# Kernel optimization log

Measured on AMD Instinct MI355X. Metric: run time of the kernel, lower is better.

Reference implementation:

```python
import jax, jax.numpy as jnp
from jax import lax
import numpy as np

C = 64      # channels
K = 3       # dynamic kernel size
N = 2       # batch
H = 256
W = 256
DOWN = 4    # avgpool factor


def _conv(x, w, b):
    # 'SAME' padding matches get_same_padding for odd kernels, dilation=1
    y = lax.conv_general_dilated(x, w, (1, 1), 'SAME',
                                 dimension_numbers=('NCHW', 'OIHW', 'NCHW'))
    return y + b[None, :, None, None]


def _resblock(x, w1, b1, w2, b2):
    out = jax.nn.leaky_relu(_conv(x, w1, b1), 0.1)
    return _conv(out, w2, b2) + x


def _block(x, ws1, bs1, ws2, bs2):
    # fixed small loop over 3 structurally distinct ResBlocks
    for i in range(ws1.shape[0]):
        x = _resblock(x, ws1[i], bs1[i], ws2[i], bs2[i])
    return x


def _avgpool(x, k):
    n, c, h, w = x.shape
    return x.reshape(n, c, h // k, k, w // k, k).mean(axis=(3, 5))


def _maxpool(x, k):
    n, c, h, w = x.shape
    return x.reshape(n, c, h // k, k, w // k, k).max(axis=(3, 5))


def _dyn_conv(x, wt, k):
    # per-pixel depthwise conv: out[n,c,h,w] = sum_{dh,dw} xpad[n,c,h+dh,w+dw] * wt[n, c*k*k + dh*k + dw, h, w]
    # (torch's unfold/permute flattening pairs feat tap (dh,dw) with kernel channel index dh*k+dw)
    n, c, h, w = x.shape
    pad = (k - 1) // 2
    xp = jnp.pad(x, ((0, 0), (0, 0), (pad, pad), (pad, pad)), mode='edge')  # replicate pad
    wr = wt.reshape(n, c, k * k, h, w)
    out = jnp.zeros_like(x)
    for dh in range(k):            # fixed 3x3 tap loop; avoids materializing the unfold tensor
        for dw in range(k):
            out = out + xp[:, :, dh:dh + h, dw:dw + w] * wr[:, :, dh * k + dw]
    return out


def setup_inputs() -> dict:
    key = jax.random.key(0)
    ks = jax.random.split(key, 11)
    s = 0.05  # small init so 6 residual blocks stay numerically tame
    return {
        'x': jax.random.normal(ks[0], (N, C, H, W), jnp.float32),
        'blk1_w1': jax.random.normal(ks[1], (3, C, C, K, K), jnp.float32) * s,
        'blk1_b1': jnp.zeros((3, C), jnp.float32),
        'blk1_w2': jax.random.normal(ks[2], (3, C, C, K, K), jnp.float32) * s,
        'blk1_b2': jnp.zeros((3, C), jnp.float32),
        'blk2_w1': jax.random.normal(ks[3], (3, C, C, K, K), jnp.float32) * s,
        'blk2_b1': jnp.zeros((3, C), jnp.float32),
        'blk2_w2': jax.random.normal(ks[4], (3, C, C, K, K), jnp.float32) * s,
        'blk2_b2': jnp.zeros((3, C), jnp.float32),
        'tok_w': jax.random.normal(ks[5], (K * K * C, C, 1, 1), jnp.float32) * s,
        'tok_b': jnp.zeros((K * K * C,), jnp.float32),
    }


def reference(x, blk1_w1, blk1_b1, blk1_w2, blk1_b2,
              blk2_w1, blk2_b1, blk2_w2, blk2_b2, tok_w, tok_b):
    y = _avgpool(x, DOWN)                                   # [N,C,H/4,W/4]
    y = _block(y, blk1_w1, blk1_b1, blk1_w2, blk1_b2)
    y = _maxpool(y, 2)                                      # [N,C,H/8,W/8]
    y = _block(y, blk2_w1, blk2_b1, blk2_w2, blk2_b2)
    wt = _conv(y, tok_w, tok_b)                             # [N,9C,H/8,W/8]
    n, ck2, hs, ws = wt.shape
    # F.interpolate(scale_factor=2*down, mode='bilinear', align_corners=False)
    wt = jax.image.resize(wt, (n, ck2, hs * 2 * DOWN, ws * 2 * DOWN), method='bilinear')
    return _dyn_conv(x, wt, K)
```

## Files before the change

### kernel.cpp

```cpp
#include <hip/hip_runtime.h>


__global__ __launch_bounds__(256) void avgpool4_k(const float* __restrict__ x,
                                                  float* __restrict__ y) {
    int idx = blockIdx.x * 256 + threadIdx.x;
    int wo = idx & 63;
    int ho = (idx >> 6) & 63;
    int cz = idx >> 12;
    const float* base = x + ((long)cz * 256 + ho * 4) * 256 + wo * 4;
    float s = 0.f;
#pragma unroll
    for (int r = 0; r < 4; ++r) {
        float4 v = *(const float4*)(base + r * 256);
        s += v.x + v.y + v.z + v.w;
    }
    y[idx] = s * 0.0625f;
}

template <int S, int CIB>
__global__ __launch_bounds__(256) void conv3x3s_k(
    const float* __restrict__ in, const float* __restrict__ wgt,
    float* __restrict__ outp) {
    constexpr int KSN = 64 / CIB;
    constexpr int TPS = S / 16;
    constexpr int NT = TPS * TPS;
    constexpr int TOT = CIB * 324;
    constexpr int NLD = (TOT + 255) / 256;
    constexpr int TAIL = TOT - (NLD - 1) * 256;
    __shared__ float s_in[CIB * 360];
    __shared__ __align__(16) float s_w[CIB * 144];

    const int tid = threadIdx.x;
    int z = blockIdx.x;
    const int ks = z % KSN; z /= KSN;
    const int ocg = z & 3; z >>= 2;
    const int tile = z % NT;
    const int n = z / NT;
    const int th = (tile / TPS) * 16, tw = (tile % TPS) * 16;
    const int oc0 = ocg * 16;

    for (int i = tid; i < CIB * 144; i += 256) {
        int k = i / (CIB * 9);
        int rem = i - k * (CIB * 9);
        s_w[rem * 16 + k] = wgt[(oc0 + k) * 576 + ks * (CIB * 9) + rem];
    }

    const float* inb = in + ((long)n * 64 + ks * CIB) * (S * S);
#pragma unroll
    for (int j = 0; j < NLD; ++j) {
        int idx = tid + j * 256;
        bool slot = (j < NLD - 1) || (tid < TAIL);
        int t = slot ? idx : 0;
        int ci = t / 324;
        int rem = t - ci * 324;
        int r = rem / 18;
        int c = rem - r * 18;
        int gh = th + r - 1, gw = tw + c - 1;
        float v = 0.f;
        if (slot && (unsigned)gh < (unsigned)S && (unsigned)gw < (unsigned)S)
            v = inb[ci * (S * S) + gh * S + gw];
        if (slot) s_in[ci * 360 + r * 20 + c] = v;
    }
    __syncthreads();

    const int lane = tid & 63;
    const int wid = tid >> 6;
    const int tx4 = (lane & 3) * 4;
    const int ty = lane >> 2;

    float acc[4][4];
#pragma unroll
    for (int k = 0; k < 4; ++k)
#pragma unroll
        for (int p = 0; p < 4; ++p) acc[k][p] = 0.f;

#pragma unroll 2
    for (int ci = 0; ci < CIB; ++ci) {
        float xr[3][6];
#pragma unroll
        for (int r = 0; r < 3; ++r) {
            const float* rp = &s_in[ci * 360 + (ty + r) * 20 + tx4];
            float4 a = *(const float4*)rp;
            float2 b = *(const float2*)(rp + 4);
            xr[r][0] = a.x; xr[r][1] = a.y; xr[r][2] = a.z;
            xr[r][3] = a.w; xr[r][4] = b.x; xr[r][5] = b.y;
        }
#pragma unroll
        for (int dh = 0; dh < 3; ++dh)
#pragma unroll
            for (int dw = 0; dw < 3; ++dw) {
                float4 wv = *(const float4*)&s_w[(ci * 9 + dh * 3 + dw) * 16 + wid * 4];
#pragma unroll
                for (int p = 0; p < 4; ++p) {
                    float xv = xr[dh][p + dw];
                    acc[0][p] += xv * wv.x;
                    acc[1][p] += xv * wv.y;
                    acc[2][p] += xv * wv.z;
                    acc[3][p] += xv * wv.w;
                }
            }
    }

    const int gy = th + ty, gx = tw + tx4;
    const long pstride = (long)2 * 64 * S * S;
#pragma unroll
    for (int k = 0; k < 4; ++k) {
        float4 v;
        v.x = acc[k][0]; v.y = acc[k][1]; v.z = acc[k][2]; v.w = acc[k][3];
        long off = ks * pstride +
                   ((long)(n * 64 + oc0 + wid * 4 + k)) * (S * S) + gy * S + gx;
        *(float4*)&outp[off] = v;
    }
}

template <int NP, int SSLOG, bool LRELU, bool RES>
__global__ __launch_bounds__(256) void comb_k(
    const float* __restrict__ P, const float* __restrict__ bias,
    const float* __restrict__ res, float* __restrict__ out) {
    const long pstride = (long)2 * 64 << SSLOG;
    long base = ((long)blockIdx.x * 256 + threadIdx.x) * 4;
    int c = (int)((base >> SSLOG) & 63);
    float4 v = *(const float4*)&P[base];
#pragma unroll
    for (int p = 1; p < NP; ++p) {
        float4 u = *(const float4*)&P[base + p * pstride];
        v.x += u.x; v.y += u.y; v.z += u.z; v.w += u.w;
    }
    float b = bias[c];
    v.x += b; v.y += b; v.z += b; v.w += b;
    if (LRELU) {
        v.x = v.x > 0.f ? v.x : 0.1f * v.x;
        v.y = v.y > 0.f ? v.y : 0.1f * v.y;
        v.z = v.z > 0.f ? v.z : 0.1f * v.z;
        v.w = v.w > 0.f ? v.w : 0.1f * v.w;
    }
    if (RES) {
        float4 r = *(const float4*)&res[base];
        v.x += r.x; v.y += r.y; v.z += r.z; v.w += r.w;
    }
    *(float4*)&out[base] = v;
}

__global__ __launch_bounds__(256) void maxpool_comb_k(
    const float* __restrict__ Pb, const float* __restrict__ bias,
    const float* __restrict__ res, float* __restrict__ P) {
    int idx = blockIdx.x * 256 + threadIdx.x;
    int wo = idx & 31;
    int ho = (idx >> 5) & 31;
    int cz = idx >> 10;
    float bch = bias[cz & 63];
    float m = -3.4e38f;
#pragma unroll
    for (int dh = 0; dh < 2; ++dh)
#pragma unroll
        for (int dw = 0; dw < 2; ++dw) {
            long off = ((long)cz * 64 + ho * 2 + dh) * 64 + wo * 2 + dw;
            float y = Pb[off] + Pb[off + 524288] + Pb[off + 1048576] +
                      Pb[off + 1572864] + bch + res[off];
            m = fmaxf(m, y);
        }
    P[idx] = m;
}

__global__ __launch_bounds__(256) void conv1x1_k(
    const float* __restrict__ in, const float* __restrict__ w,
    const float* __restrict__ b, float* __restrict__ out) {
    __shared__ float s_in[32 * 256];
    __shared__ __align__(16) float s_w[64 * 8];
    const int tid = threadIdx.x;
    const int p0 = blockIdx.x * 256;
    const int cog = blockIdx.y;
    const int n = blockIdx.z;

    for (int idx = tid; idx < 512; idx += 256) {
        int j = idx >> 6;
        int ci = idx & 63;
        s_w[ci * 8 + j] = w[(long)cog * 512 + idx];
    }

    float acc[8];
#pragma unroll
    for (int i = 0; i < 8; ++i) acc[i] = b[cog * 8 + i];

    float pf[32];
#pragma unroll
    for (int i = 0; i < 32; ++i)
        pf[i] = in[(long)(n * 64 + i) * 1024 + p0 + tid];

    for (int chunk = 0; chunk < 64; chunk += 32) {
        __syncthreads();
#pragma unroll
        for (int i = 0; i < 32; ++i) s_in[i * 256 + tid] = pf[i];
        __syncthreads();
        if (chunk + 32 < 64) {
#pragma unroll
            for (int i = 0; i < 32; ++i)
                pf[i] = in[(long)(n * 64 + chunk + 32 + i) * 1024 + p0 + tid];
        }
#pragma unroll 4
        for (int ci = 0; ci < 32; ++ci) {
            float v = s_in[ci * 256 + tid];
            float4 w0 = *(const float4*)&s_w[(chunk + ci) * 8];
            float4 w1 = *(const float4*)&s_w[(chunk + ci) * 8 + 4];
            acc[0] += v * w0.x; acc[1] += v * w0.y;
            acc[2] += v * w0.z; acc[3] += v * w0.w;
            acc[4] += v * w1.x; acc[5] += v * w1.y;
            acc[6] += v * w1.z; acc[7] += v * w1.w;
        }
    }
#pragma unroll
    for (int oc = 0; oc < 8; ++oc)
        out[(long)(n * 576 + cog * 8 + oc) * 1024 + p0 + tid] = acc[oc];
}

__global__ __launch_bounds__(256) void dynconv_k(
    const float* __restrict__ x, const float* __restrict__ wt,
    float* __restrict__ out) {
    __shared__ __align__(16) float s_x[10 * 132];
    const int tid = threadIdx.x;
    const int tx = tid & 31;
    const int ty = tid >> 5;
    const int tw = (blockIdx.x & 1) * 128;
    const int th = (blockIdx.x >> 1) * 8;
    const int cz = blockIdx.y;

    const float* xb = x + (long)cz * 65536;
    for (int idx = tid; idx < 1300; idx += 256) {
        int r = idx / 130;
        int c = idx - r * 130;
        int gh = min(max(th + r - 1, 0), 255);
        int gw = min(max(tw + c - 1, 0), 255);
        s_x[r * 132 + c] = xb[gh * 256 + gw];
    }

    const int h = th + ty;
    const int wbase = tw + tx * 4;

    float src_h = h * 0.125f - 0.4375f;
    int h0 = (int)floorf(src_h);
    float fh = src_h - (float)h0;
    int h0c = min(max(h0, 0), 31), h1c = min(max(h0 + 1, 0), 31);
    float src_w = wbase * 0.125f - 0.4375f;
    int w0 = (int)floorf(src_w);
    float fw0 = src_w - (float)w0;
    int w0c = min(max(w0, 0), 31), w1c = min(max(w0 + 1, 0), 31);

    __syncthreads();

    float vals[3][6];
#pragma unroll
    for (int r = 0; r < 3; ++r) {
        const float* rp = &s_x[(ty + r) * 132 + tx * 4];
        float4 a = *(const float4*)rp;
        float2 b = *(const float2*)(rp + 4);
        vals[r][0] = a.x; vals[r][1] = a.y; vals[r][2] = a.z;
        vals[r][3] = a.w; vals[r][4] = b.x; vals[r][5] = b.y;
    }

    const float* wtb = wt + (long)cz * 9 * 1024;
    float acc[4] = {0.f, 0.f, 0.f, 0.f};
#pragma unroll
    for (int dh = 0; dh < 3; ++dh)
#pragma unroll
        for (int dw = 0; dw < 3; ++dw) {
            const float* p = wtb + (dh * 3 + dw) * 1024;
            float w00 = p[h0c * 32 + w0c], w01 = p[h0c * 32 + w1c];
            float w10 = p[h1c * 32 + w0c], w11 = p[h1c * 32 + w1c];
            float c0 = w00 + fh * (w10 - w00);
            float c1 = w01 + fh * (w11 - w01);
            float d = c1 - c0;
#pragma unroll
            for (int j = 0; j < 4; ++j) {
                float wv = c0 + (fw0 + 0.125f * j) * d;
                acc[j] += vals[dh][j + dw] * wv;
            }
        }

    float4 o;
    o.x = acc[0]; o.y = acc[1]; o.z = acc[2]; o.w = acc[3];
    *(float4*)&out[(long)cz * 65536 + h * 256 + wbase] = o;
}

extern "C" void kernel_launch(void* const* d_in, const int* in_sizes, int n_in,
                              void* d_out, int out_size, void* d_ws, size_t ws_size,
                              hipStream_t stream) {
    const float* x    = (const float*)d_in[0];
    const float* b1w1 = (const float*)d_in[1];
    const float* b1b1 = (const float*)d_in[2];
    const float* b1w2 = (const float*)d_in[3];
    const float* b1b2 = (const float*)d_in[4];
    const float* b2w1 = (const float*)d_in[5];
    const float* b2b1 = (const float*)d_in[6];
    const float* b2w2 = (const float*)d_in[7];
    const float* b2b2 = (const float*)d_in[8];
    const float* tokw = (const float*)d_in[9];
    const float* tokb = (const float*)d_in[10];
    float* out = (float*)d_out;
    float* ws = (float*)d_ws;

    float* X0 = ws;
    float* X1 = ws + 524288;
    float* T  = ws + 1048576;
    float* P  = ws + 1572864;
    float* Pm = ws + 3670016;
    float* Q  = ws + 3801088;
    float* U  = ws + 3932160;
    float* WT = ws + 4063232;

    const int WSZ = 64 * 64 * 9;

    avgpool4_k<<<2048, 256, 0, stream>>>(x, X0);

    conv3x3s_k<64, 16><<<512, 256, 0, stream>>>(X0, b1w1 + 0 * WSZ, P);
    comb_k<4, 12, true,  false><<<512, 256, 0, stream>>>(P, b1b1 + 0, nullptr, T);
    conv3x3s_k<64, 16><<<512, 256, 0, stream>>>(T, b1w2 + 0 * WSZ, P);
    comb_k<4, 12, false, true ><<<512, 256, 0, stream>>>(P, b1b2 + 0, X0, X1);

    conv3x3s_k<64, 16><<<512, 256, 0, stream>>>(X1, b1w1 + 1 * WSZ, P);
    comb_k<4, 12, true,  false><<<512, 256, 0, stream>>>(P, b1b1 + 64, nullptr, T);
    conv3x3s_k<64, 16><<<512, 256, 0, stream>>>(T, b1w2 + 1 * WSZ, P);
    comb_k<4, 12, false, true ><<<512, 256, 0, stream>>>(P, b1b2 + 64, X1, X0);

    conv3x3s_k<64, 16><<<512, 256, 0, stream>>>(X0, b1w1 + 2 * WSZ, P);
    comb_k<4, 12, true,  false><<<512, 256, 0, stream>>>(P, b1b1 + 128, nullptr, T);
    conv3x3s_k<64, 16><<<512, 256, 0, stream>>>(T, b1w2 + 2 * WSZ, P);
    maxpool_comb_k<<<512, 256, 0, stream>>>(P, b1b2 + 128, X0, Pm);

    conv3x3s_k<32, 8><<<256, 256, 0, stream>>>(Pm, b2w1 + 0 * WSZ, P);
    comb_k<8, 10, true,  false><<<128, 256, 0, stream>>>(P, b2b1 + 0, nullptr, U);
    conv3x3s_k<32, 8><<<256, 256, 0, stream>>>(U, b2w2 + 0 * WSZ, P);
    comb_k<8, 10, false, true ><<<128, 256, 0, stream>>>(P, b2b2 + 0, Pm, Q);

    conv3x3s_k<32, 8><<<256, 256, 0, stream>>>(Q, b2w1 + 1 * WSZ, P);
    comb_k<8, 10, true,  false><<<128, 256, 0, stream>>>(P, b2b1 + 64, nullptr, U);
    conv3x3s_k<32, 8><<<256, 256, 0, stream>>>(U, b2w2 + 1 * WSZ, P);
    comb_k<8, 10, false, true ><<<128, 256, 0, stream>>>(P, b2b2 + 64, Q, Pm);

    conv3x3s_k<32, 8><<<256, 256, 0, stream>>>(Pm, b2w1 + 2 * WSZ, P);
    comb_k<8, 10, true,  false><<<128, 256, 0, stream>>>(P, b2b1 + 128, nullptr, U);
    conv3x3s_k<32, 8><<<256, 256, 0, stream>>>(U, b2w2 + 2 * WSZ, P);
    comb_k<8, 10, false, true ><<<128, 256, 0, stream>>>(P, b2b2 + 128, Pm, Q);

    conv1x1_k<<<dim3(4, 72, 2), 256, 0, stream>>>(Q, tokw, tokb, WT);

    dynconv_k<<<dim3(64, 128), 256, 0, stream>>>(x, WT, out);
}
```

Measured before the change: 387.9 us.

## Widen conv tiles, deepen split-K, and stage dynconv weights in shared memory

```diff
diff --git a/kernel.cpp b/kernel.cpp
--- a/kernel.cpp
+++ b/kernel.cpp
@@ -17,17 +17,20 @@
     y[idx] = s * 0.0625f;
 }
 
-template <int S, int CIB>
-__global__ __launch_bounds__(256) void conv3x3s_k(
+template <int S, int CIB, int TW, int PXL>
+__global__ __launch_bounds__(256) void conv3x3w_k(
     const float* __restrict__ in, const float* __restrict__ wgt,
     float* __restrict__ outp) {
     constexpr int KSN = 64 / CIB;
-    constexpr int TPS = S / 16;
-    constexpr int NT = TPS * TPS;
-    constexpr int TOT = CIB * 324;
+    constexpr int TH = 16;
+    constexpr int NTW = S / TW, NTH = S / TH;
+    constexpr int NT = NTW * NTH;
+    constexpr int HW = TW + 2;
+    constexpr int SROW = TW + 4;
+    constexpr int TOT = CIB * 18 * HW;
     constexpr int NLD = (TOT + 255) / 256;
     constexpr int TAIL = TOT - (NLD - 1) * 256;
-    __shared__ float s_in[CIB * 360];
+    __shared__ float s_in[CIB * 18 * SROW];
     __shared__ __align__(16) float s_w[CIB * 144];
 
     const int tid = threadIdx.x;
@@ -36,7 +39,7 @@
     const int ocg = z & 3; z >>= 2;
     const int tile = z % NT;
     const int n = z / NT;
-    const int th = (tile / TPS) * 16, tw = (tile % TPS) * 16;
+    const int th0 = (tile / NTW) * TH, tw0 = (tile % NTW) * TW;
     const int oc0 = ocg * 16;
 
     for (int i = tid; i < CIB * 144; i += 256) {
@@ -51,39 +54,44 @@
         int idx = tid + j * 256;
         bool slot = (j < NLD - 1) || (tid < TAIL);
         int t = slot ? idx : 0;
-        int ci = t / 324;
-        int rem = t - ci * 324;
-        int r = rem / 18;
-        int c = rem - r * 18;
-        int gh = th + r - 1, gw = tw + c - 1;
+        int ci = t / (18 * HW);
+        int rem = t - ci * (18 * HW);
+        int r = rem / HW;
+        int c = rem - r * HW;
+        int gh = th0 + r - 1, gw = tw0 + c - 1;
         float v = 0.f;
         if (slot && (unsigned)gh < (unsigned)S && (unsigned)gw < (unsigned)S)
             v = inb[ci * (S * S) + gh * S + gw];
-        if (slot) s_in[ci * 360 + r * 20 + c] = v;
+        if (slot) s_in[ci * (18 * SROW) + r * SROW + c] = v;
     }
     __syncthreads();
 
     const int lane = tid & 63;
     const int wid = tid >> 6;
-    const int tx4 = (lane & 3) * 4;
-    const int ty = lane >> 2;
-
-    float acc[4][4];
+    const int lx = lane & 3;
+    const int ly = lane >> 2;
+    const int px0 = lx * PXL;
+
+    float acc[4][PXL];
 #pragma unroll
     for (int k = 0; k < 4; ++k)
 #pragma unroll
-        for (int p = 0; p < 4; ++p) acc[k][p] = 0.f;
-
-#pragma unroll 2
+        for (int p = 0; p < PXL; ++p) acc[k][p] = 0.f;
+
+#pragma unroll
     for (int ci = 0; ci < CIB; ++ci) {
-        float xr[3][6];
+        float xr[3][PXL + 2];
 #pragma unroll
         for (int r = 0; r < 3; ++r) {
-            const float* rp = &s_in[ci * 360 + (ty + r) * 20 + tx4];
-            float4 a = *(const float4*)rp;
-            float2 b = *(const float2*)(rp + 4);
-            xr[r][0] = a.x; xr[r][1] = a.y; xr[r][2] = a.z;
-            xr[r][3] = a.w; xr[r][4] = b.x; xr[r][5] = b.y;
+            const float* rp = &s_in[ci * (18 * SROW) + (ly + r) * SROW + px0];
+#pragma unroll
+            for (int q = 0; q < PXL / 4; ++q) {
+                float4 a = *(const float4*)(rp + q * 4);
+                xr[r][q * 4 + 0] = a.x; xr[r][q * 4 + 1] = a.y;
+                xr[r][q * 4 + 2] = a.z; xr[r][q * 4 + 3] = a.w;
+            }
+            float2 b = *(const float2*)(rp + PXL);
+            xr[r][PXL] = b.x; xr[r][PXL + 1] = b.y;
         }
 #pragma unroll
         for (int dh = 0; dh < 3; ++dh)
@@ -91,7 +99,7 @@
             for (int dw = 0; dw < 3; ++dw) {
                 float4 wv = *(const float4*)&s_w[(ci * 9 + dh * 3 + dw) * 16 + wid * 4];
 #pragma unroll
-                for (int p = 0; p < 4; ++p) {
+                for (int p = 0; p < PXL; ++p) {
                     float xv = xr[dh][p + dw];
                     acc[0][p] += xv * wv.x;
                     acc[1][p] += xv * wv.y;
@@ -101,15 +109,19 @@
             }
     }
 
-    const int gy = th + ty, gx = tw + tx4;
+    const int gy = th0 + ly, gx = tw0 + px0;
     const long pstride = (long)2 * 64 * S * S;
 #pragma unroll
     for (int k = 0; k < 4; ++k) {
-        float4 v;
-        v.x = acc[k][0]; v.y = acc[k][1]; v.z = acc[k][2]; v.w = acc[k][3];
         long off = ks * pstride +
                    ((long)(n * 64 + oc0 + wid * 4 + k)) * (S * S) + gy * S + gx;
-        *(float4*)&outp[off] = v;
+#pragma unroll
+        for (int q = 0; q < PXL / 4; ++q) {
+            float4 v;
+            v.x = acc[k][q * 4 + 0]; v.y = acc[k][q * 4 + 1];
+            v.z = acc[k][q * 4 + 2]; v.w = acc[k][q * 4 + 3];
+            *(float4*)&outp[off + q * 4] = v;
+        }
     }
 }
 
@@ -141,6 +153,7 @@
     *(float4*)&out[base] = v;
 }
 
+template <int NP>
 __global__ __launch_bounds__(256) void maxpool_comb_k(
     const float* __restrict__ Pb, const float* __restrict__ bias,
     const float* __restrict__ res, float* __restrict__ P) {
@@ -155,8 +168,9 @@
 #pragma unroll
         for (int dw = 0; dw < 2; ++dw) {
             long off = ((long)cz * 64 + ho * 2 + dh) * 64 + wo * 2 + dw;
-            float y = Pb[off] + Pb[off + 524288] + Pb[off + 1048576] +
-                      Pb[off + 1572864] + bch + res[off];
+            float y = bch + res[off];
+#pragma unroll
+            for (int p = 0; p < NP; ++p) y += Pb[off + (long)p * 524288];
             m = fmaxf(m, y);
         }
     P[idx] = m;
@@ -217,6 +231,7 @@
     const float* __restrict__ x, const float* __restrict__ wt,
     float* __restrict__ out) {
     __shared__ __align__(16) float s_x[10 * 132];
+    __shared__ float s_wt[9 * 60];
     const int tid = threadIdx.x;
     const int tx = tid & 31;
     const int ty = tid >> 5;
@@ -233,17 +248,31 @@
         s_x[r * 132 + c] = xb[gh * 256 + gw];
     }
 
+    const int h0min = th / 8 - 1;
+    const int w0min = tw / 8 - 1;
+    const float* wtb = wt + (long)cz * 9 * 1024;
+    for (int i = tid; i < 540; i += 256) {
+        int tap = i / 60;
+        int rem = i - tap * 60;
+        int r = rem / 20;
+        int c = rem - r * 20;
+        if (c < 18) {
+            int gr = min(max(h0min + r, 0), 31);
+            int gc = min(max(w0min + c, 0), 31);
+            s_wt[i] = wtb[tap * 1024 + gr * 32 + gc];
+        }
+    }
+
     const int h = th + ty;
     const int wbase = tw + tx * 4;
-
     float src_h = h * 0.125f - 0.4375f;
     int h0 = (int)floorf(src_h);
     float fh = src_h - (float)h0;
-    int h0c = min(max(h0, 0), 31), h1c = min(max(h0 + 1, 0), 31);
+    int r0 = h0 - h0min;
     float src_w = wbase * 0.125f - 0.4375f;
     int w0 = (int)floorf(src_w);
     float fw0 = src_w - (float)w0;
-    int w0c = min(max(w0, 0), 31), w1c = min(max(w0 + 1, 0), 31);
+    int j = w0 - w0min;
 
     __syncthreads();
 
@@ -257,22 +286,21 @@
         vals[r][3] = a.w; vals[r][4] = b.x; vals[r][5] = b.y;
     }
 
-    const float* wtb = wt + (long)cz * 9 * 1024;
     float acc[4] = {0.f, 0.f, 0.f, 0.f};
 #pragma unroll
     for (int dh = 0; dh < 3; ++dh)
 #pragma unroll
         for (int dw = 0; dw < 3; ++dw) {
-            const float* p = wtb + (dh * 3 + dw) * 1024;
-            float w00 = p[h0c * 32 + w0c], w01 = p[h0c * 32 + w1c];
-            float w10 = p[h1c * 32 + w0c], w11 = p[h1c * 32 + w1c];
-            float c0 = w00 + fh * (w10 - w00);
-            float c1 = w01 + fh * (w11 - w01);
+            const float* p = &s_wt[(dh * 3 + dw) * 60 + r0 * 20 + j];
+            float t0 = p[0], t1 = p[1];
+            float b0 = p[20], b1 = p[21];
+            float c0 = t0 + fh * (b0 - t0);
+            float c1 = t1 + fh * (b1 - t1);
             float d = c1 - c0;
 #pragma unroll
-            for (int j = 0; j < 4; ++j) {
-                float wv = c0 + (fw0 + 0.125f * j) * d;
-                acc[j] += vals[dh][j + dw] * wv;
+            for (int jj = 0; jj < 4; ++jj) {
+                float wv = c0 + (fw0 + 0.125f * jj) * d;
+                acc[jj] += vals[dh][jj + dw] * wv;
             }
         }
 
@@ -302,44 +330,44 @@
     float* X1 = ws + 524288;
     float* T  = ws + 1048576;
     float* P  = ws + 1572864;
-    float* Pm = ws + 3670016;
-    float* Q  = ws + 3801088;
-    float* U  = ws + 3932160;
-    float* WT = ws + 4063232;
+    float* Pm = ws + 5767168;
+    float* Q  = ws + 5898240;
+    float* U  = ws + 6029312;
+    float* WT = ws + 6160384;
 
     const int WSZ = 64 * 64 * 9;
 
     avgpool4_k<<<2048, 256, 0, stream>>>(x, X0);
 
-    conv3x3s_k<64, 16><<<512, 256, 0, stream>>>(X0, b1w1 + 0 * WSZ, P);
-    comb_k<4, 12, true,  false><<<512, 256, 0, stream>>>(P, b1b1 + 0, nullptr, T);
-    conv3x3s_k<64, 16><<<512, 256, 0, stream>>>(T, b1w2 + 0 * WSZ, P);
-    comb_k<4, 12, false, true ><<<512, 256, 0, stream>>>(P, b1b2 + 0, X0, X1);
-
-    conv3x3s_k<64, 16><<<512, 256, 0, stream>>>(X1, b1w1 + 1 * WSZ, P);
-    comb_k<4, 12, true,  false><<<512, 256, 0, stream>>>(P, b1b1 + 64, nullptr, T);
-    conv3x3s_k<64, 16><<<512, 256, 0, stream>>>(T, b1w2 + 1 * WSZ, P);
-    comb_k<4, 12, false, true ><<<512, 256, 0, stream>>>(P, b1b2 + 64, X1, X0);
-
-    conv3x3s_k<64, 16><<<512, 256, 0, stream>>>(X0, b1w1 + 2 * WSZ, P);
-    comb_k<4, 12, true,  false><<<512, 256, 0, stream>>>(P, b1b1 + 128, nullptr, T);
-    conv3x3s_k<64, 16><<<512, 256, 0, stream>>>(T, b1w2 + 2 * WSZ, P);
-    maxpool_comb_k<<<512, 256, 0, stream>>>(P, b1b2 + 128, X0, Pm);
-
-    conv3x3s_k<32, 8><<<256, 256, 0, stream>>>(Pm, b2w1 + 0 * WSZ, P);
-    comb_k<8, 10, true,  false><<<128, 256, 0, stream>>>(P, b2b1 + 0, nullptr, U);
-    conv3x3s_k<32, 8><<<256, 256, 0, stream>>>(U, b2w2 + 0 * WSZ, P);
-    comb_k<8, 10, false, true ><<<128, 256, 0, stream>>>(P, b2b2 + 0, Pm, Q);
-
-    conv3x3s_k<32, 8><<<256, 256, 0, stream>>>(Q, b2w1 + 1 * WSZ, P);
-    comb_k<8, 10, true,  false><<<128, 256, 0, stream>>>(P, b2b1 + 64, nullptr, U);
-    conv3x3s_k<32, 8><<<256, 256, 0, stream>>>(U, b2w2 + 1 * WSZ, P);
-    comb_k<8, 10, false, true ><<<128, 256, 0, stream>>>(P, b2b2 + 64, Q, Pm);
-
-    conv3x3s_k<32, 8><<<256, 256, 0, stream>>>(Pm, b2w1 + 2 * WSZ, P);
-    comb_k<8, 10, true,  false><<<128, 256, 0, stream>>>(P, b2b1 + 128, nullptr, U);
-    conv3x3s_k<32, 8><<<256, 256, 0, stream>>>(U, b2w2 + 2 * WSZ, P);
-    comb_k<8, 10, false, true ><<<128, 256, 0, stream>>>(P, b2b2 + 128, Pm, Q);
+    conv3x3w_k<64, 8, 32, 8><<<512, 256, 0, stream>>>(X0, b1w1 + 0 * WSZ, P);
+    comb_k<8, 12, true,  false><<<512, 256, 0, stream>>>(P, b1b1 + 0, nullptr, T);
+    conv3x3w_k<64, 8, 32, 8><<<512, 256, 0, stream>>>(T, b1w2 + 0 * WSZ, P);
+    comb_k<8, 12, false, true ><<<512, 256, 0, stream>>>(P, b1b2 + 0, X0, X1);
+
+    conv3x3w_k<64, 8, 32, 8><<<512, 256, 0, stream>>>(X1, b1w1 + 1 * WSZ, P);
+    comb_k<8, 12, true,  false><<<512, 256, 0, stream>>>(P, b1b1 + 64, nullptr, T);
+    conv3x3w_k<64, 8, 32, 8><<<512, 256, 0, stream>>>(T, b1w2 + 1 * WSZ, P);
+    comb_k<8, 12, false, true ><<<512, 256, 0, stream>>>(P, b1b2 + 64, X1, X0);
+
+    conv3x3w_k<64, 8, 32, 8><<<512, 256, 0, stream>>>(X0, b1w1 + 2 * WSZ, P);
+    comb_k<8, 12, true,  false><<<512, 256, 0, stream>>>(P, b1b1 + 128, nullptr, T);
+    conv3x3w_k<64, 8, 32, 8><<<512, 256, 0, stream>>>(T, b1w2 + 2 * WSZ, P);
+    maxpool_comb_k<8><<<512, 256, 0, stream>>>(P, b1b2 + 128, X0, Pm);
+
+    conv3x3w_k<32, 4, 16, 4><<<512, 256, 0, stream>>>(Pm, b2w1 + 0 * WSZ, P);
+    comb_k<16, 10, true,  false><<<128, 256, 0, stream>>>(P, b2b1 + 0, nullptr, U);
+    conv3x3w_k<32, 4, 16, 4><<<512, 256, 0, stream>>>(U, b2w2 + 0 * WSZ, P);
+    comb_k<16, 10, false, true ><<<128, 256, 0, stream>>>(P, b2b2 + 0, Pm, Q);
+
+    conv3x3w_k<32, 4, 16, 4><<<512, 256, 0, stream>>>(Q, b2w1 + 1 * WSZ, P);
+    comb_k<16, 10, true,  false><<<128, 256, 0, stream>>>(P, b2b1 + 64, nullptr, U);
+    conv3x3w_k<32, 4, 16, 4><<<512, 256, 0, stream>>>(U, b2w2 + 1 * WSZ, P);
+    comb_k<16, 10, false, true ><<<128, 256, 0, stream>>>(P, b2b2 + 64, Q, Pm);
+
+    conv3x3w_k<32, 4, 16, 4><<<512, 256, 0, stream>>>(Pm, b2w1 + 2 * WSZ, P);
+    comb_k<16, 10, true,  false><<<128, 256, 0, stream>>>(P, b2b1 + 128, nullptr, U);
+    conv3x3w_k<32, 4, 16, 4><<<512, 256, 0, stream>>>(U, b2w2 + 2 * WSZ, P);
+    comb_k<16, 10, false, true ><<<128, 256, 0, stream>>>(P, b2b2 + 128, Pm, Q);
 
     conv1x1_k<<<dim3(4, 72, 2), 256, 0, stream>>>(Q, tokw, tokb, WT);
 
```

After: 369.3 us. 1.05x faster.
